# Performance work log

Measured on AMD Instinct MI355X. Metric: run time of the kernel, lower is better.

Reference implementation:

```python
import jax, jax.numpy as jnp
import numpy as np


def setup_inputs() -> dict:
    key = jax.random.key(0)
    k1, k2, k3 = jax.random.split(key, 3)
    B, S, N, C, H = 4, 12, 4096, 64, 128
    x = jax.random.normal(k1, (B, S, N, C), dtype=jnp.float32)
    A = jax.random.uniform(k2, (N, N), dtype=jnp.float32)
    W_emb = jax.random.normal(k3, (H, C), dtype=jnp.float32) * 0.05  # nn.Linear weight [out,in]
    return {"x": x, "A": A, "W_emb": W_emb}


def reference(x, A, W_emb):
    # x: [B,S,N,C], A: [N,N], W_emb: [H,C]
    x_emb = jnp.einsum('bsnc,hc->bsnh', x, W_emb)  # Linear(bias=False)
    d = (jnp.sum(A, axis=-1) + 1.0) ** (-0.5)      # diag of D_tilde, [N]
    N = A.shape[0]
    # L_tilde = I - D_tilde @ A @ D_tilde (diag matmuls == row/col scaling)
    L_tilde = jnp.eye(N, dtype=A.dtype) - d[:, None] * A * d[None, :]
    H = jnp.einsum('ik,bskj->bsij', L_tilde, x_emb)
    out = jax.nn.sigmoid(H)
    return (out, A)
```

## Files before the change

### kernel.cpp

```cpp
#include <hip/hip_runtime.h>
#include <hip/hip_bf16.h>
#include <stdint.h>

typedef __attribute__((ext_vector_type(8))) short short8;
typedef __attribute__((ext_vector_type(4))) float floatx4;

#define N_NODES 4096
#define CDIM 64
#define HDIM 128

#define AS1 __attribute__((address_space(1)))
#define AS3 __attribute__((address_space(3)))

__device__ __forceinline__ void gload_lds16(const void* g, void* l) {
    __builtin_amdgcn_global_load_lds((const AS1 void*)g, (AS3 void*)l, 16, 0, 0);
}

#define SB0 __builtin_amdgcn_sched_barrier(0)
#define BARRIER __builtin_amdgcn_s_barrier()
#define LGKM0 asm volatile("s_waitcnt lgkmcnt(0)" ::: "memory")

__global__ __launch_bounds__(256) void k_prep(const float* __restrict__ A,
                                              float* __restrict__ outA,
                                              __hip_bfloat16* __restrict__ Ab,
                                              float* __restrict__ dvec) {
    const int row = blockIdx.x;
    const int t = threadIdx.x;
    const float4* Ar = (const float4*)(A + (size_t)row * N_NODES);
    float4* Or = (float4*)(outA + (size_t)row * N_NODES);
    short4* Br = (short4*)(Ab + (size_t)row * N_NODES);
    float s = 0.f;
    #pragma unroll
    for (int j = 0; j < 4; ++j) {
        int q = t + j * 256;
        float4 v = Ar[q];
        Or[q] = v;
        union { __hip_bfloat16 h[4]; short4 s4; } u;
        u.h[0] = __float2bfloat16(v.x);
        u.h[1] = __float2bfloat16(v.y);
        u.h[2] = __float2bfloat16(v.z);
        u.h[3] = __float2bfloat16(v.w);
        Br[q] = u.s4;
        s += v.x + v.y + v.z + v.w;
    }
    #pragma unroll
    for (int off = 32; off > 0; off >>= 1) s += __shfl_down(s, off, 64);
    __shared__ float ps[4];
    if ((t & 63) == 0) ps[t >> 6] = s;
    __syncthreads();
    if (t == 0) {
        float tot = ps[0] + ps[1] + ps[2] + ps[3];
        dvec[row] = rsqrtf(tot + 1.0f);
    }
}

__global__ __launch_bounds__(256) void k_buildXt(const float* __restrict__ x,
                                                 const float* __restrict__ dvec,
                                                 __hip_bfloat16* __restrict__ Xt) {
    __shared__ float tile[64 * 65];
    __shared__ float dloc[64];
    const int t = threadIdx.x;
    const int bs = blockIdx.y;
    const int k0 = blockIdx.x * 64;
    const float* xp = x + ((size_t)bs * N_NODES + k0) * CDIM;
    const float4* xp4 = (const float4*)xp;
    #pragma unroll
    for (int it = 0; it < 4; ++it) {
        int q = it * 256 + t;
        float4 v = xp4[q];
        int p = q * 4;
        int kk = p >> 6, c = p & 63;
        tile[kk * 65 + c + 0] = v.x;
        tile[kk * 65 + c + 1] = v.y;
        tile[kk * 65 + c + 2] = v.z;
        tile[kk * 65 + c + 3] = v.w;
    }
    if (t < 64) dloc[t] = dvec[k0 + t];
    __syncthreads();
    #pragma unroll
    for (int it = 0; it < 16; ++it) {
        int p = it * 256 + t;
        int c = p >> 6;
        int kk = p & 63;
        float v = tile[kk * 65 + c] * dloc[kk];
        Xt[(size_t)(bs * CDIM + c) * N_NODES + k0 + kk] = __float2bfloat16(v);
    }
}

__global__ __launch_bounds__(512, 2) void k_gemm_out(const __hip_bfloat16* __restrict__ Ab,
                                                     const __hip_bfloat16* __restrict__ Xt,
                                                     const float* __restrict__ x,
                                                     const float* __restrict__ dvec,
                                                     const float* __restrict__ W,
                                                     float* __restrict__ out) {
    __shared__ __align__(16) char smem[149504];
    __hip_bfloat16* Wbs = (__hip_bfloat16*)(smem + 131072);

    const int t = threadIdx.x;
    const int w = t >> 6, l = t & 63;
    const int wm = w >> 2, wn = w & 3;
    const int ar = l & 15;
    const int kq = (l >> 4) * 8;
    const int kqb = kq * 2;
    const int col = l & 15;
    const int rowq = (l >> 4) * 4;
    const int xorR = ((ar >> 1) & 3) << 4;

    const int flat = blockIdx.x;
    const int tid2 = (flat & 7) * 24 + (flat >> 3);
    const int bx = tid2 % 12;
    const int by = tid2 / 12;
    const int i0 = by * 256;
    const int j0 = bx * 256;

    {
        const float4* W4 = (const float4*)W;
        #pragma unroll
        for (int it = 0; it < 4; ++it) {
            int q4 = it * 512 + t;
            float4 v = W4[q4];
            int p = q4 * 4;
            int h = p >> 6, c = p & 63;
            union { __hip_bfloat16 hh[4]; short4 s4; } u;
            u.hh[0] = __float2bfloat16(v.x);
            u.hh[1] = __float2bfloat16(v.y);
            u.hh[2] = __float2bfloat16(v.z);
            u.hh[3] = __float2bfloat16(v.w);
            *(short4*)(Wbs + h * 72 + c) = u.s4;
        }
    }
    SB0;

    const int rloc = w * 16 + (l >> 2);
    const int slot = (l & 3) ^ ((rloc >> 1) & 3);
    const __hip_bfloat16* gA = Ab + (size_t)(i0 + rloc) * N_NODES + slot * 8;
    const __hip_bfloat16* gB = Xt + (size_t)(j0 + rloc) * N_NODES + slot * 8;

    auto stage = [&](const __hip_bfloat16* gbase, int buf, int subByte, int tile, int kk) {
        const __hip_bfloat16* g = gbase + tile * 64 + kk * 32;
        char* d = smem + buf * 65536 + subByte + w * 1024;
        gload_lds16(g, d);
        gload_lds16(g + (size_t)128 * N_NODES, d + 8192);
    };

    floatx4 acc[8][4];
    #pragma unroll
    for (int a = 0; a < 8; ++a)
        #pragma unroll
        for (int b = 0; b < 4; ++b)
            acc[a][b] = (floatx4){0.f, 0.f, 0.f, 0.f};

    auto ldA = [&](short8* dst, int buf, int kk, int mh) {
        const char* base = smem + buf * 65536 + kk * 16384;
        const int off = (wm * 128 + mh * 64 + ar) * 64 + (kqb ^ xorR);
        #pragma unroll
        for (int mt = 0; mt < 4; ++mt)
            dst[mt] = *(const short8*)(base + off + mt * 1024);
    };
    auto ldB = [&](short8* dst, int buf, int kk) {
        const char* base = smem + buf * 65536 + 32768 + kk * 16384;
        const int off = (wn * 64 + ar) * 64 + (kqb ^ xorR);
        #pragma unroll
        for (int nt = 0; nt < 4; ++nt)
            dst[nt] = *(const short8*)(base + off + nt * 1024);
    };
    auto mm16 = [&](const short8* a, const short8* b, int mh) {
        #pragma unroll
        for (int mt = 0; mt < 4; ++mt)
            #pragma unroll
            for (int nt = 0; nt < 4; ++nt)
                acc[mh * 4 + mt][nt] = __builtin_amdgcn_mfma_f32_16x16x32_bf16(
                    a[mt], b[nt], acc[mh * 4 + mt][nt], 0, 0, 0);
    };

    stage(gA, 0, 0,     0, 0);
    stage(gB, 0, 32768, 0, 0);
    stage(gA, 0, 16384, 0, 1);
    stage(gB, 0, 49152, 0, 1);
    stage(gB, 1, 32768, 1, 0);
    stage(gA, 1, 0,     1, 0);
    stage(gB, 1, 49152, 1, 1);
    asm volatile("s_waitcnt vmcnt(6)" ::: "memory");
    BARRIER;

    #pragma unroll 2
    for (int tt = 0; tt < 64; ++tt) {
        const int buf = tt & 1;
        short8 a4[4], b4[4];

        SB0;
        ldA(a4, buf, 0, 0); ldB(b4, buf, 0);
        SB0;
        if (tt + 1 < 64) stage(gA, buf ^ 1, 16384, tt + 1, 1);
        BARRIER; LGKM0; SB0;
        __builtin_amdgcn_s_setprio(1);
        mm16(a4, b4, 0);
        __builtin_amdgcn_s_setprio(0);
        BARRIER;

        SB0;
        ldA(a4, buf, 0, 1);
        SB0;
        if (tt + 2 < 64) stage(gB, buf, 32768, tt + 2, 0);
        BARRIER; LGKM0; SB0;
        __builtin_amdgcn_s_setprio(1);
        mm16(a4, b4, 1);
        __builtin_amdgcn_s_setprio(0);
        BARRIER;

        SB0;
        ldA(a4, buf, 1, 0); ldB(b4, buf, 1);
        SB0;
        if (tt + 2 < 64) stage(gA, buf, 0, tt + 2, 0);
        BARRIER; LGKM0; SB0;
        __builtin_amdgcn_s_setprio(1);
        mm16(a4, b4, 0);
        __builtin_amdgcn_s_setprio(0);
        BARRIER;

        SB0;
        ldA(a4, buf, 1, 1);
        SB0;
        if (tt + 2 < 64) stage(gB, buf, 49152, tt + 2, 1);
        BARRIER; LGKM0; SB0;
        __builtin_amdgcn_s_setprio(1);
        mm16(a4, b4, 1);
        __builtin_amdgcn_s_setprio(0);
        if (tt < 62) { asm volatile("s_waitcnt vmcnt(6)" ::: "memory"); }
        else         { asm volatile("s_waitcnt vmcnt(0)" ::: "memory"); }
        BARRIER;
    }

    const int bx4 = bx * 4;
    #pragma unroll
    for (int am = 0; am < 8; ++am) {
        const int irel = wm * 128 + am * 16 + rowq;
        float dv[4];
        #pragma unroll
        for (int r = 0; r < 4; ++r) dv[r] = dvec[i0 + irel + r];
        #pragma unroll
        for (int nt = 0; nt < 4; ++nt) {
            const int c = nt * 16 + col;
            const size_t xbase = ((size_t)(bx4 + wn) * N_NODES + i0 + irel) * CDIM + c;
            #pragma unroll
            for (int r = 0; r < 4; ++r) {
                const int row = irel + r;
                float g = x[xbase + (size_t)r * CDIM] - dv[r] * acc[am][nt][r];
                *(__hip_bfloat16*)(smem + wn * 32768 + row * 128 +
                                   ((c * 2) ^ ((row & 7) << 4))) = __float2bfloat16(g);
            }
        }
    }
    __syncthreads();

    const int bsr2 = w >> 1, ihalf = w & 1;
    const size_t obase = (size_t)(bx4 + bsr2) * N_NODES + i0 + ihalf * 128;
    #pragma unroll
    for (int hh = 0; hh < 2; ++hh) {
        floatx4 o[8][4];
        #pragma unroll
        for (int a = 0; a < 8; ++a)
            #pragma unroll
            for (int b = 0; b < 4; ++b)
                o[a][b] = (floatx4){0.f, 0.f, 0.f, 0.f};
        #pragma unroll
        for (int ks = 0; ks < 2; ++ks) {
            short8 gf[8], wf[4];
            const int kb = ks * 64 + kqb;
            #pragma unroll
            for (int mt = 0; mt < 8; ++mt) {
                const int grow = ihalf * 128 + mt * 16 + ar;
                gf[mt] = *(const short8*)(smem + bsr2 * 32768 + grow * 128 +
                                          (kb ^ ((grow & 7) << 4)));
            }
            #pragma unroll
            for (int nt = 0; nt < 4; ++nt) {
                const int hrow = hh * 64 + nt * 16 + ar;
                wf[nt] = *(const short8*)(Wbs + hrow * 72 + ks * 32 + kq);
            }
            #pragma unroll
            for (int mt = 0; mt < 8; ++mt)
                #pragma unroll
                for (int nt = 0; nt < 4; ++nt)
                    o[mt][nt] = __builtin_amdgcn_mfma_f32_16x16x32_bf16(
                        gf[mt], wf[nt], o[mt][nt], 0, 0, 0);
        }
        #pragma unroll
        for (int mt = 0; mt < 8; ++mt) {
            #pragma unroll
            for (int nt = 0; nt < 4; ++nt) {
                const int h = hh * 64 + nt * 16 + col;
                #pragma unroll
                for (int r = 0; r < 4; ++r) {
                    const size_t i = obase + mt * 16 + rowq + r;
                    out[i * HDIM + h] = 1.f / (1.f + __expf(-o[mt][nt][r]));
                }
            }
        }
    }
}

__global__ __launch_bounds__(256) void k_gemm(const __hip_bfloat16* __restrict__ Ab,
                                              const __hip_bfloat16* __restrict__ Xt,
                                              const float* __restrict__ x,
                                              const float* __restrict__ dvec,
                                              __hip_bfloat16* __restrict__ G) {
    __shared__ __hip_bfloat16 As[128 * 32];
    __shared__ __hip_bfloat16 Bs[128 * 32];
    const int t = threadIdx.x;
    const int w = t >> 6, l = t & 63;
    const int i0 = blockIdx.y * 128;
    const int j0 = blockIdx.x * 128;
    const int wm = w >> 1, wn = w & 1;
    const int ar = l & 15;
    const int kq = (l >> 4) * 8;
    const int srow = t >> 2;
    const int skcol = (t & 3) * 8;

    floatx4 acc[4][4];
    #pragma unroll
    for (int a = 0; a < 4; ++a)
        #pragma unroll
        for (int b = 0; b < 4; ++b)
            acc[a][b] = (floatx4){0.f, 0.f, 0.f, 0.f};

    const __hip_bfloat16* gA0 = Ab + (size_t)(i0 + srow) * N_NODES + skcol;
    const __hip_bfloat16* gB0 = Xt + (size_t)(j0 + srow) * N_NODES + skcol;

    for (int k0 = 0; k0 < N_NODES; k0 += 32) {
        __syncthreads();
        gload_lds16(gA0 + k0,                        As + w * 512);
        gload_lds16(gA0 + (size_t)64 * N_NODES + k0, As + 2048 + w * 512);
        gload_lds16(gB0 + k0,                        Bs + w * 512);
        gload_lds16(gB0 + (size_t)64 * N_NODES + k0, Bs + 2048 + w * 512);
        __syncthreads();
        short8 af[4], bfr[4];
        #pragma unroll
        for (int mt = 0; mt < 4; ++mt)
            af[mt] = *(const short8*)(As + (wm * 64 + mt * 16 + ar) * 32 + kq);
        #pragma unroll
        for (int nt = 0; nt < 4; ++nt)
            bfr[nt] = *(const short8*)(Bs + (wn * 64 + nt * 16 + ar) * 32 + kq);
        #pragma unroll
        for (int mt = 0; mt < 4; ++mt)
            #pragma unroll
            for (int nt = 0; nt < 4; ++nt)
                acc[mt][nt] = __builtin_amdgcn_mfma_f32_16x16x32_bf16(
                    af[mt], bfr[nt], acc[mt][nt], 0, 0, 0);
    }

    #pragma unroll
    for (int mt = 0; mt < 4; ++mt) {
        const int ibase = i0 + wm * 64 + mt * 16 + (l >> 4) * 4;
        #pragma unroll
        for (int nt = 0; nt < 4; ++nt) {
            const int j = j0 + wn * 64 + nt * 16 + (l & 15);
            const int bs = j >> 6, c = j & 63;
            #pragma unroll
            for (int r = 0; r < 4; ++r) {
                const int i = ibase + r;
                const size_t xi = ((size_t)bs * N_NODES + i) * CDIM + c;
                float g = x[xi] - dvec[i] * acc[mt][nt][r];
                G[xi] = __float2bfloat16(g);
            }
        }
    }
}

__global__ __launch_bounds__(256) void k_out(const __hip_bfloat16* __restrict__ G,
                                             const float* __restrict__ W,
                                             float* __restrict__ out) {
    __shared__ float Wt[64 * 132];
    __shared__ __hip_bfloat16 Gs[32 * 64];
    const int t = threadIdx.x;
    const int bs = blockIdx.y;
    const int i0 = blockIdx.x * 32;
    #pragma unroll
    for (int it = 0; it < 32; ++it) {
        int p = it * 256 + t;
        int h = p & 127, c = p >> 7;
        Wt[c * 132 + h] = W[h * 64 + c];
    }
    const short4* gp4 = (const short4*)(G + ((size_t)bs * N_NODES + i0) * CDIM);
    ((short4*)Gs)[t]       = gp4[t];
    ((short4*)Gs)[256 + t] = gp4[256 + t];
    __syncthreads();

    const int hg = t & 31;
    const int ig = t >> 5;
    float acc[4][4] = {};
    #pragma unroll
    for (int c = 0; c < 64; ++c) {
        float4 wv = *(const float4*)(Wt + c * 132 + hg * 4);
        #pragma unroll
        for (int ii = 0; ii < 4; ++ii) {
            float g = __bfloat162float(Gs[(ig * 4 + ii) * 64 + c]);
            acc[ii][0] += g * wv.x;
            acc[ii][1] += g * wv.y;
            acc[ii][2] += g * wv.z;
            acc[ii][3] += g * wv.w;
        }
    }
    #pragma unroll
    for (int ii = 0; ii < 4; ++ii) {
        const int i = i0 + ig * 4 + ii;
        float4 o;
        o.x = 1.f / (1.f + __expf(-acc[ii][0]));
        o.y = 1.f / (1.f + __expf(-acc[ii][1]));
        o.z = 1.f / (1.f + __expf(-acc[ii][2]));
        o.w = 1.f / (1.f + __expf(-acc[ii][3]));
        *(float4*)(out + ((size_t)bs * N_NODES + i) * HDIM + hg * 4) = o;
    }
}

extern "C" void kernel_launch(void* const* d_in, const int* in_sizes, int n_in,
                              void* d_out, int out_size, void* d_ws, size_t ws_size,
                              hipStream_t stream) {
    const float* x = (const float*)d_in[0];
    const float* A = (const float*)d_in[1];
    const float* W = (const float*)d_in[2];
    float* out  = (float*)d_out;
    float* outA = out + 25165824;

    char* ws = (char*)d_ws;
    float* dvec = (float*)ws;
    const size_t offD = 16384;
    const size_t szAb = (size_t)16777216 * 2;
    const size_t szXt = (size_t)3072 * 4096 * 2;

    if (ws_size >= offD + szAb + szXt) {
        __hip_bfloat16* Ab = (__hip_bfloat16*)(ws + offD);
        __hip_bfloat16* Xt = (__hip_bfloat16*)(ws + offD + szAb);
        k_prep    <<<4096, 256, 0, stream>>>(A, outA, Ab, dvec);
        k_buildXt <<<dim3(64, 48), 256, 0, stream>>>(x, dvec, Xt);
        k_gemm_out<<<192, 512, 0, stream>>>(Ab, Xt, x, dvec, W, out);
    } else {
        __hip_bfloat16* Ab = (__hip_bfloat16*)out;
        __hip_bfloat16* Xt = (__hip_bfloat16*)(ws + offD);
        __hip_bfloat16* G  = (__hip_bfloat16*)(ws + offD + szXt);
        k_prep    <<<4096, 256, 0, stream>>>(A, outA, Ab, dvec);
        k_buildXt <<<dim3(64, 48), 256, 0, stream>>>(x, dvec, Xt);
        k_gemm    <<<dim3(24, 32), 256, 0, stream>>>(Ab, Xt, x, dvec, G);
        k_out     <<<dim3(128, 48), 256, 0, stream>>>(G, W, out);
    }
}
```

Measured before the change: 374.0 us.

## Retile fused GEMM to 256x192 tiles so grid fills all 256 CUs

Changes the fused GEMM+projection kernel's N-tile from 256 to 192 columns, growing the grid from 192 to 256 workgroups so every CU on the MI355X gets one block. The B tile is restaged as one 64-wide K chunk per buffer with a new XOR swizzle and three loads per wave, and the LDS footprint shrinks. The epilogue maps 192 columns to three batch-step slices, and only six of eight waves run the W projection. The aim is better CU occupancy, at the cost of a lower MFMA-to-load ratio per tile and two idle waves in the epilogue.

```diff
diff --git a/kernel.cpp b/kernel.cpp
--- a/kernel.cpp
+++ b/kernel.cpp
@@ -93,8 +93,8 @@
                                                      const float* __restrict__ dvec,
                                                      const float* __restrict__ W,
                                                      float* __restrict__ out) {
-    __shared__ __align__(16) char smem[149504];
-    __hip_bfloat16* Wbs = (__hip_bfloat16*)(smem + 131072);
+    __shared__ __align__(16) char smem[133120];
+    __hip_bfloat16* Wbs = (__hip_bfloat16*)(smem + 114688);
 
     const int t = threadIdx.x;
     const int w = t >> 6, l = t & 63;
@@ -104,14 +104,15 @@
     const int kqb = kq * 2;
     const int col = l & 15;
     const int rowq = (l >> 4) * 4;
-    const int xorR = ((ar >> 1) & 3) << 4;
+    const int xorA = ((ar >> 1) & 3) << 4;
+    const int xorB = (ar & 7) << 4;
 
     const int flat = blockIdx.x;
-    const int tid2 = (flat & 7) * 24 + (flat >> 3);
-    const int bx = tid2 % 12;
-    const int by = tid2 / 12;
+    const int tid2 = (flat & 7) * 32 + (flat >> 3);
+    const int bx = tid2 & 15;
+    const int by = tid2 >> 4;
     const int i0 = by * 256;
-    const int j0 = bx * 256;
+    const int j0 = bx * 192;
 
     {
         const float4* W4 = (const float4*)W;
@@ -132,106 +133,115 @@
     SB0;
 
     const int rloc = w * 16 + (l >> 2);
-    const int slot = (l & 3) ^ ((rloc >> 1) & 3);
-    const __hip_bfloat16* gA = Ab + (size_t)(i0 + rloc) * N_NODES + slot * 8;
-    const __hip_bfloat16* gB = Xt + (size_t)(j0 + rloc) * N_NODES + slot * 8;
-
-    auto stage = [&](const __hip_bfloat16* gbase, int buf, int subByte, int tile, int kk) {
-        const __hip_bfloat16* g = gbase + tile * 64 + kk * 32;
-        char* d = smem + buf * 65536 + subByte + w * 1024;
+    const int slotA = (l & 3) ^ ((rloc >> 1) & 3);
+    const __hip_bfloat16* gA = Ab + (size_t)(i0 + rloc) * N_NODES + slotA * 8;
+
+    auto stageA = [&](int buf, int kk, int tile) {
+        const __hip_bfloat16* g = gA + tile * 64 + kk * 32;
+        char* d = smem + buf * 32768 + kk * 16384 + w * 1024;
         gload_lds16(g, d);
         gload_lds16(g + (size_t)128 * N_NODES, d + 8192);
     };
 
-    floatx4 acc[8][4];
+    const int brow_l = l >> 3;
+    const int bchunk = (l & 7) ^ brow_l;
+    const __hip_bfloat16* gB = Xt + (size_t)(j0 + brow_l) * N_NODES + bchunk * 8;
+
+    auto stageB = [&](int buf, int tile) {
+        #pragma unroll
+        for (int i = 0; i < 3; ++i) {
+            const int seg = 3 * w + i;
+            gload_lds16(gB + (size_t)(8 * seg) * N_NODES + tile * 64,
+                        smem + 65536 + buf * 24576 + seg * 1024);
+        }
+    };
+
+    floatx4 acc[8][3];
     #pragma unroll
     for (int a = 0; a < 8; ++a)
         #pragma unroll
-        for (int b = 0; b < 4; ++b)
+        for (int b = 0; b < 3; ++b)
             acc[a][b] = (floatx4){0.f, 0.f, 0.f, 0.f};
 
     auto ldA = [&](short8* dst, int buf, int kk, int mh) {
-        const char* base = smem + buf * 65536 + kk * 16384;
-        const int off = (wm * 128 + mh * 64 + ar) * 64 + (kqb ^ xorR);
+        const char* base = smem + buf * 32768 + kk * 16384;
+        const int off = (wm * 128 + mh * 64 + ar) * 64 + (kqb ^ xorA);
         #pragma unroll
         for (int mt = 0; mt < 4; ++mt)
             dst[mt] = *(const short8*)(base + off + mt * 1024);
     };
     auto ldB = [&](short8* dst, int buf, int kk) {
-        const char* base = smem + buf * 65536 + 32768 + kk * 16384;
-        const int off = (wn * 64 + ar) * 64 + (kqb ^ xorR);
-        #pragma unroll
-        for (int nt = 0; nt < 4; ++nt)
-            dst[nt] = *(const short8*)(base + off + nt * 1024);
+        const char* base = smem + 65536 + buf * 24576;
+        const int off = (wn * 48 + ar) * 128 + ((kk * 64 + kqb) ^ xorB);
+        #pragma unroll
+        for (int nt = 0; nt < 3; ++nt)
+            dst[nt] = *(const short8*)(base + off + nt * 2048);
     };
-    auto mm16 = [&](const short8* a, const short8* b, int mh) {
+    auto mm12 = [&](const short8* a, const short8* b, int mh) {
         #pragma unroll
         for (int mt = 0; mt < 4; ++mt)
             #pragma unroll
-            for (int nt = 0; nt < 4; ++nt)
+            for (int nt = 0; nt < 3; ++nt)
                 acc[mh * 4 + mt][nt] = __builtin_amdgcn_mfma_f32_16x16x32_bf16(
                     a[mt], b[nt], acc[mh * 4 + mt][nt], 0, 0, 0);
     };
 
-    stage(gA, 0, 0,     0, 0);
-    stage(gB, 0, 32768, 0, 0);
-    stage(gA, 0, 16384, 0, 1);
-    stage(gB, 0, 49152, 0, 1);
-    stage(gB, 1, 32768, 1, 0);
-    stage(gA, 1, 0,     1, 0);
-    stage(gB, 1, 49152, 1, 1);
-    asm volatile("s_waitcnt vmcnt(6)" ::: "memory");
+    stageA(0, 0, 0);
+    stageA(0, 1, 0);
+    stageB(0, 0);
+    stageA(1, 0, 1);
+    stageB(1, 1);
+    asm volatile("s_waitcnt vmcnt(5)" ::: "memory");
     BARRIER;
 
     #pragma unroll 2
     for (int tt = 0; tt < 64; ++tt) {
         const int buf = tt & 1;
-        short8 a4[4], b4[4];
-
-        SB0;
-        ldA(a4, buf, 0, 0); ldB(b4, buf, 0);
-        SB0;
-        if (tt + 1 < 64) stage(gA, buf ^ 1, 16384, tt + 1, 1);
+        short8 a4[4], b3[3];
+
+        SB0;
+        ldA(a4, buf, 0, 0); ldB(b3, buf, 0);
+        SB0;
+        if (tt + 1 < 64) stageA(buf ^ 1, 1, tt + 1);
         BARRIER; LGKM0; SB0;
         __builtin_amdgcn_s_setprio(1);
-        mm16(a4, b4, 0);
+        mm12(a4, b3, 0);
         __builtin_amdgcn_s_setprio(0);
         BARRIER;
 
         SB0;
         ldA(a4, buf, 0, 1);
         SB0;
-        if (tt + 2 < 64) stage(gB, buf, 32768, tt + 2, 0);
         BARRIER; LGKM0; SB0;
         __builtin_amdgcn_s_setprio(1);
-        mm16(a4, b4, 1);
+        mm12(a4, b3, 1);
         __builtin_amdgcn_s_setprio(0);
         BARRIER;
 
         SB0;
-        ldA(a4, buf, 1, 0); ldB(b4, buf, 1);
-        SB0;
-        if (tt + 2 < 64) stage(gA, buf, 0, tt + 2, 0);
+        ldA(a4, buf, 1, 0); ldB(b3, buf, 1);
+        SB0;
+        if (tt + 2 < 64) stageA(buf, 0, tt + 2);
         BARRIER; LGKM0; SB0;
         __builtin_amdgcn_s_setprio(1);
-        mm16(a4, b4, 0);
+        mm12(a4, b3, 0);
         __builtin_amdgcn_s_setprio(0);
         BARRIER;
 
         SB0;
         ldA(a4, buf, 1, 1);
         SB0;
-        if (tt + 2 < 64) stage(gB, buf, 49152, tt + 2, 1);
+        if (tt + 2 < 64) stageB(buf, tt + 2);
         BARRIER; LGKM0; SB0;
         __builtin_amdgcn_s_setprio(1);
-        mm16(a4, b4, 1);
+        mm12(a4, b3, 1);
         __builtin_amdgcn_s_setprio(0);
-        if (tt < 62) { asm volatile("s_waitcnt vmcnt(6)" ::: "memory"); }
+        if (tt < 62) { asm volatile("s_waitcnt vmcnt(5)" ::: "memory"); }
         else         { asm volatile("s_waitcnt vmcnt(0)" ::: "memory"); }
         BARRIER;
     }
 
-    const int bx4 = bx * 4;
+    const int bx3 = bx * 3;
     #pragma unroll
     for (int am = 0; am < 8; ++am) {
         const int irel = wm * 128 + am * 16 + rowq;
@@ -239,61 +249,64 @@
         #pragma unroll
         for (int r = 0; r < 4; ++r) dv[r] = dvec[i0 + irel + r];
         #pragma unroll
-        for (int nt = 0; nt < 4; ++nt) {
-            const int c = nt * 16 + col;
-            const size_t xbase = ((size_t)(bx4 + wn) * N_NODES + i0 + irel) * CDIM + c;
+        for (int nt = 0; nt < 3; ++nt) {
+            const int jrel = wn * 48 + nt * 16 + col;
+            const int bsr = jrel >> 6, c = jrel & 63;
+            const size_t xbase = ((size_t)(bx3 + bsr) * N_NODES + i0 + irel) * CDIM + c;
             #pragma unroll
             for (int r = 0; r < 4; ++r) {
                 const int row = irel + r;
                 float g = x[xbase + (size_t)r * CDIM] - dv[r] * acc[am][nt][r];
-                *(__hip_bfloat16*)(smem + wn * 32768 + row * 128 +
+                *(__hip_bfloat16*)(smem + bsr * 32768 + row * 128 +
                                    ((c * 2) ^ ((row & 7) << 4))) = __float2bfloat16(g);
             }
         }
     }
     __syncthreads();
 
-    const int bsr2 = w >> 1, ihalf = w & 1;
-    const size_t obase = (size_t)(bx4 + bsr2) * N_NODES + i0 + ihalf * 128;
-    #pragma unroll
-    for (int hh = 0; hh < 2; ++hh) {
-        floatx4 o[8][4];
-        #pragma unroll
-        for (int a = 0; a < 8; ++a)
-            #pragma unroll
-            for (int b = 0; b < 4; ++b)
-                o[a][b] = (floatx4){0.f, 0.f, 0.f, 0.f};
-        #pragma unroll
-        for (int ks = 0; ks < 2; ++ks) {
-            short8 gf[8], wf[4];
-            const int kb = ks * 64 + kqb;
+    if (w < 6) {
+        const int bsr2 = w >> 1, ihalf = w & 1;
+        const size_t obase = (size_t)(bx3 + bsr2) * N_NODES + i0 + ihalf * 128;
+        #pragma unroll
+        for (int hh = 0; hh < 2; ++hh) {
+            floatx4 o[8][4];
+            #pragma unroll
+            for (int a = 0; a < 8; ++a)
+                #pragma unroll
+                for (int b = 0; b < 4; ++b)
+                    o[a][b] = (floatx4){0.f, 0.f, 0.f, 0.f};
+            #pragma unroll
+            for (int ks = 0; ks < 2; ++ks) {
+                short8 gf[8], wf[4];
+                const int kb = ks * 64 + kqb;
+                #pragma unroll
+                for (int mt = 0; mt < 8; ++mt) {
+                    const int grow = ihalf * 128 + mt * 16 + ar;
+                    gf[mt] = *(const short8*)(smem + bsr2 * 32768 + grow * 128 +
+                                              (kb ^ ((grow & 7) << 4)));
+                }
+                #pragma unroll
+                for (int nt = 0; nt < 4; ++nt) {
+                    const int hrow = hh * 64 + nt * 16 + ar;
+                    wf[nt] = *(const short8*)(Wbs + hrow * 72 + ks * 32 + kq);
+                }
+                #pragma unroll
+                for (int mt = 0; mt < 8; ++mt)
+                    #pragma unroll
+                    for (int nt = 0; nt < 4; ++nt)
+                        o[mt][nt] = __builtin_amdgcn_mfma_f32_16x16x32_bf16(
+                            gf[mt], wf[nt], o[mt][nt], 0, 0, 0);
+            }
             #pragma unroll
             for (int mt = 0; mt < 8; ++mt) {
-                const int grow = ihalf * 128 + mt * 16 + ar;
-                gf[mt] = *(const short8*)(smem + bsr2 * 32768 + grow * 128 +
-                                          (kb ^ ((grow & 7) << 4)));
-            }
-            #pragma unroll
-            for (int nt = 0; nt < 4; ++nt) {
-                const int hrow = hh * 64 + nt * 16 + ar;
-                wf[nt] = *(const short8*)(Wbs + hrow * 72 + ks * 32 + kq);
-            }
-            #pragma unroll
-            for (int mt = 0; mt < 8; ++mt)
                 #pragma unroll
-                for (int nt = 0; nt < 4; ++nt)
-                    o[mt][nt] = __builtin_amdgcn_mfma_f32_16x16x32_bf16(
-                        gf[mt], wf[nt], o[mt][nt], 0, 0, 0);
-        }
-        #pragma unroll
-        for (int mt = 0; mt < 8; ++mt) {
-            #pragma unroll
-            for (int nt = 0; nt < 4; ++nt) {
-                const int h = hh * 64 + nt * 16 + col;
-                #pragma unroll
-                for (int r = 0; r < 4; ++r) {
-                    const size_t i = obase + mt * 16 + rowq + r;
-                    out[i * HDIM + h] = 1.f / (1.f + __expf(-o[mt][nt][r]));
+                for (int nt = 0; nt < 4; ++nt) {
+                    const int h = hh * 64 + nt * 16 + col;
+                    #pragma unroll
+                    for (int r = 0; r < 4; ++r) {
+                        const size_t i = obase + mt * 16 + rowq + r;
+                        out[i * HDIM + h] = 1.f / (1.f + __expf(-o[mt][nt][r]));
+                    }
                 }
             }
         }
@@ -433,7 +446,7 @@
         __hip_bfloat16* Xt = (__hip_bfloat16*)(ws + offD + szAb);
         k_prep    <<<4096, 256, 0, stream>>>(A, outA, Ab, dvec);
         k_buildXt <<<dim3(64, 48), 256, 0, stream>>>(x, dvec, Xt);
-        k_gemm_out<<<192, 512, 0, stream>>>(Ab, Xt, x, dvec, W, out);
+        k_gemm_out<<<256, 512, 0, stream>>>(Ab, Xt, x, dvec, W, out);
     } else {
         __hip_bfloat16* Ab = (__hip_bfloat16*)out;
         __hip_bfloat16* Xt = (__hip_bfloat16*)(ws + offD);
```

After: 355.5 us. -4.9%, faster.
